# Performance work log

Hardware: AMD Instinct MI355X
Metric: run time of the kernel (lower is better)

## Reference

```python
import jax, jax.numpy as jnp
import numpy as np

E = 8       # num experts
T = 1024    # num tokens
H = 1024    # hidden dim
I = 1024    # intermediate dim (per gate/up half)


def setup_inputs() -> dict:
    key = jax.random.key(0)
    k1, k2, k3, k4 = jax.random.split(key, 4)
    return {
        "hidden_states": jax.random.normal(k1, (T, H), jnp.float32),
        "router_logits": jax.random.normal(k2, (T, E), jnp.float32),
        # W13 stored pre-transposed as in the module: [E, H, 2*I]
        "W13": jax.random.normal(k3, (E, H, 2 * I), jnp.float32) * 0.02,
        # W2 stored pre-transposed: [E, I, H]
        "W2": jax.random.normal(k4, (E, I, H), jnp.float32) * 0.02,
        "top_k": 2,
    }


def reference(hidden_states, router_logits, W13, W2, top_k):
    num_experts = router_logits.shape[-1]
    # --- routing: topk_softmax (softmax over all experts, then top-k) ---
    probs = jax.nn.softmax(router_logits, axis=-1)            # [T, E]
    w, idx = jax.lax.top_k(probs, top_k)                      # [T, K]
    # renormalize=True path of moe_gather
    w = w / jnp.sum(w, axis=-1, keepdims=True)
    # combine weights per expert: [T, E]
    combine = jnp.sum(jax.nn.one_hot(idx, num_experts, dtype=w.dtype) * w[..., None], axis=1)
    # --- grouped gate-up GEMM + silu_and_mul ---
    h13 = jnp.einsum('th,ehf->tef', hidden_states, W13)       # [T, E, 2I]
    gate, up = jnp.split(h13, 2, axis=-1)                     # each [T, E, I]
    act = jax.nn.silu(gate) * up                              # silu_and_mul
    # --- grouped down GEMM ---
    down = jnp.einsum('tei,eih->teh', act, W2)                # [T, E, H]
    # --- combine (moe_gather) ---
    return jnp.einsum('te,teh->th', combine, down)            # [T, H]
```

## Files before the change

kernel.cpp:

```cpp
#include <hip/hip_runtime.h>
#include <stdint.h>

#define NE    8
#define NTOK  1024
#define NH    1024
#define NI    1024
#define N13   2048

#define PREP_BLOCKS 6657
#define G1MAX       768
#define G2MAX       768

typedef __attribute__((ext_vector_type(8))) short short8;
typedef __attribute__((ext_vector_type(4))) float f32x4;
typedef unsigned short u16;
typedef unsigned int   u32;

__device__ __forceinline__ u16 f2bf(float x) {
    union { float f; u32 u; } v; v.f = x;
    return (u16)((v.u + 0x7fffu + ((v.u >> 16) & 1u)) >> 16);
}
__device__ __forceinline__ u32 cvt_pk(float lo, float hi) {
    u32 r;
    asm("v_cvt_pk_bf16_f32 %0, %1, %2" : "=v"(r) : "v"(lo), "v"(hi));
    return r;
}
__device__ __forceinline__ void async_ld16(u16* lds, const u16* g) {
    __builtin_amdgcn_global_load_lds(
        (const __attribute__((address_space(1))) u32*)g,
        (__attribute__((address_space(3))) u32*)lds, 16, 0, 0);
}

__device__ __forceinline__ bool find_tile(
    const int* __restrict__ counts, int tile, int bm, int ntn,
    int& e_o, int& mt_o, int& nt_o, int& cnt_o, int& base_o)
{
    int base = 0;
    #pragma unroll
    for (int e = 0; e < NE; e++) {
        const int cnt = counts[e];
        const int mtiles = (cnt + bm - 1) / bm;
        const int tiles = mtiles * ntn;
        if (tile < tiles) {
            e_o = e; mt_o = tile / ntn; nt_o = tile - (tile / ntn) * ntn;
            cnt_o = cnt; base_o = base; return true;
        }
        tile -= tiles; base += cnt;
    }
    return false;
}

#define SYNCV(N)                                                           \
    {                                                                      \
        asm volatile("s_waitcnt vmcnt(" #N ") lgkmcnt(0)" ::: "memory");   \
        __builtin_amdgcn_s_barrier();                                      \
        __builtin_amdgcn_sched_barrier(0);                                 \
    }

__global__ __launch_bounds__(256) void prep_kernel(
    const float* __restrict__ X, const float* __restrict__ logits,
    const float* __restrict__ W13, const float* __restrict__ W2,
    int* __restrict__ counts, int* __restrict__ pair_tok,
    int* __restrict__ inv, float* __restrict__ tokw,
    u16* __restrict__ Xb, u16* __restrict__ W13t, u16* __restrict__ W2t)
{
    __shared__ __align__(16) float Ts[64][65];
    const int tid = threadIdx.x;
    const int b = blockIdx.x;

    if (b == 0) {
        int* s_cnt  = (int*)&Ts[0][0];
        int* s_base = s_cnt + NE;
        if (tid < NE) s_cnt[tid] = 0;
        __syncthreads();
        int eA[4][2]; int slotA[4][2]; float wA[4][2];
        #pragma unroll
        for (int i = 0; i < 4; i++) {
            const int t = tid * 4 + i;
            float l[NE];
            #pragma unroll
            for (int e = 0; e < NE; e++) l[e] = logits[t * NE + e];
            int i0 = 0;
            #pragma unroll
            for (int e = 1; e < NE; e++) if (l[e] > l[i0]) i0 = e;
            int i1 = -1;
            #pragma unroll
            for (int e = 0; e < NE; e++) {
                if (e == i0) continue;
                if (i1 < 0 || l[e] > l[i1]) i1 = e;
            }
            const float e10 = __expf(l[i1] - l[i0]);
            const float invw = 1.0f / (1.0f + e10);
            eA[i][0] = i0; eA[i][1] = i1;
            wA[i][0] = invw; wA[i][1] = e10 * invw;
            slotA[i][0] = atomicAdd(&s_cnt[i0], 1);
            slotA[i][1] = atomicAdd(&s_cnt[i1], 1);
        }
        __syncthreads();
        if (tid == 0) {
            int acc = 0;
            #pragma unroll
            for (int e = 0; e < NE; e++) { s_base[e] = acc; acc += s_cnt[e]; }
        }
        __syncthreads();
        if (tid < NE) counts[tid] = s_cnt[tid];
        #pragma unroll
        for (int i = 0; i < 4; i++) {
            const int t = tid * 4 + i;
            #pragma unroll
            for (int k = 0; k < 2; k++) {
                const int p = s_base[eA[i][k]] + slotA[i][k];
                pair_tok[p] = t;
                inv[t * 2 + k] = p;
                tokw[t * 2 + k] = wA[i][k];
            }
        }
    } else if (b <= 512) {
        const int i = (b - 1) * 256 + tid;
        const float4* s = (const float4*)X;
        const float4 a = s[2 * i], c = s[2 * i + 1];
        uint4 o;
        o.x = cvt_pk(a.x, a.y);
        o.y = cvt_pk(a.z, a.w);
        o.z = cvt_pk(c.x, c.y);
        o.w = cvt_pk(c.z, c.w);
        *(uint4*)(Xb + (size_t)i * 8) = o;
    } else {
        const int wb = b - 513;
        const float* src; u16* dst; int K, N, tb;
        if (wb < 4096) { src = W13; dst = W13t; K = NH; N = N13; tb = wb; }
        else           { src = W2;  dst = W2t;  K = NI; N = NH;  tb = wb - 4096; }
        const int ktiles = K >> 6, ntiles = N >> 6;
        const int tpe = ktiles * ntiles;
        const int e = tb / tpe;
        const int rem = tb - e * tpe;
        const int kt = rem / ntiles, ntl = rem - (rem / ntiles) * ntiles;
        const float* sb = src + ((size_t)e * K + (size_t)kt * 64) * N + ntl * 64;
        #pragma unroll
        for (int i = 0; i < 4; i++) {
            const int idx = tid + i * 256;
            const int r = idx >> 4, c = (idx & 15) << 2;
            const float4 v = *(const float4*)(sb + (size_t)r * N + c);
            Ts[r][c + 0] = v.x; Ts[r][c + 1] = v.y;
            Ts[r][c + 2] = v.z; Ts[r][c + 3] = v.w;
        }
        __syncthreads();
        u16* db = dst + ((size_t)e * N + (size_t)ntl * 64) * K + kt * 64;
        #pragma unroll
        for (int i = 0; i < 2; i++) {
            const int u = tid + i * 256;
            const int n = u >> 3, k8 = (u & 7) << 3;
            uint4 o;
            o.x = cvt_pk(Ts[k8 + 0][n], Ts[k8 + 1][n]);
            o.y = cvt_pk(Ts[k8 + 2][n], Ts[k8 + 3][n]);
            o.z = cvt_pk(Ts[k8 + 4][n], Ts[k8 + 5][n]);
            o.w = cvt_pk(Ts[k8 + 6][n], Ts[k8 + 7][n]);
            *(uint4*)(db + (size_t)n * K + k8) = o;
        }
    }
}

__global__ __launch_bounds__(256, 3) void gemm1_kernel(
    const u16* __restrict__ Xb, const u16* __restrict__ W13t,
    const int* __restrict__ counts, const int* __restrict__ pair_tok,
    u16* __restrict__ act)
{
    int e, mt, nt, cnt, base;
    if (!find_tile(counts, blockIdx.x, 128, 32, e, mt, nt, cnt, base)) return;

    __shared__ __align__(16) u16 As[4][128 * 32];
    __shared__ __align__(16) u16 Bs[4][64 * 32];

    const int tid = threadIdx.x;
    const int ct  = nt * 32;

    const int sc = (((tid & 3) ^ ((tid >> 3) & 3)) << 3);
    const int rr = tid >> 2;
    const int tok0 = pair_tok[base + min(mt * 128 + rr,      cnt - 1)];
    const int tok1 = pair_tok[base + min(mt * 128 + 64 + rr, cnt - 1)];
    const u16* ga0 = Xb + (size_t)tok0 * NH + sc;
    const u16* ga1 = Xb + (size_t)tok1 * NH + sc;
    const int wcol = (rr < 32) ? (ct + rr) : (NI + ct + rr - 32);
    const u16* gb  = W13t + ((size_t)e * N13 + wcol) * NH + sc;

    const int lane = tid & 63, w = tid >> 6;
    const int quad = lane >> 4, lid = lane & 15;
    const int rw = w >> 1, cw = w & 1;
    int aoff[4];
    #pragma unroll
    for (int mi = 0; mi < 4; mi++) {
        const int row = rw * 64 + mi * 16 + lid;
        aoff[mi] = row * 32 + ((quad ^ ((row >> 1) & 3)) << 3);
    }
    int bgoff, buoff;
    { const int n = cw * 16 + lid;
      bgoff = n * 32 + ((quad ^ ((n >> 1) & 3)) << 3); }
    { const int n = 32 + cw * 16 + lid;
      buoff = n * 32 + ((quad ^ ((n >> 1) & 3)) << 3); }

    f32x4 accg[4] = {};
    f32x4 accu[4] = {};

#define STAGE1(S, K)                                                       \
    {                                                                      \
        async_ld16(&As[S][tid * 8],         ga0 + (K));                    \
        async_ld16(&As[S][(256 + tid) * 8], ga1 + (K));                    \
        async_ld16(&Bs[S][tid * 8],         gb  + (K));                    \
    }
#define COMP1(S)                                                           \
    {                                                                      \
        const short8 gv = *(const short8*)&Bs[S][bgoff];                   \
        const short8 uv = *(const short8*)&Bs[S][buoff];                   \
        __builtin_amdgcn_s_setprio(1);                                     \
        _Pragma("unroll") for (int mi = 0; mi < 4; mi++) {                 \
            const short8 av = *(const short8*)&As[S][aoff[mi]];            \
            accg[mi] = __builtin_amdgcn_mfma_f32_16x16x32_bf16(            \
                av, gv, accg[mi], 0, 0, 0);                                \
            accu[mi] = __builtin_amdgcn_mfma_f32_16x16x32_bf16(            \
                av, uv, accu[mi], 0, 0, 0);                                \
        }                                                                  \
        __builtin_amdgcn_s_setprio(0);                                     \
    }
#define STEP1(J, NV)                                                       \
    SYNCV(NV)                                                              \
    if ((J) + 3 < 32) { STAGE1((((J) + 3) & 3), (((J) + 3) * 32)) }        \
    COMP1(((J) & 3))

    STAGE1(0, 0)
    STAGE1(1, 32)
    STAGE1(2, 64)

    STEP1(0, 6)  STEP1(1, 6)  STEP1(2, 6)  STEP1(3, 6)
    STEP1(4, 6)  STEP1(5, 6)  STEP1(6, 6)  STEP1(7, 6)
    STEP1(8, 6)  STEP1(9, 6)  STEP1(10, 6) STEP1(11, 6)
    STEP1(12, 6) STEP1(13, 6) STEP1(14, 6) STEP1(15, 6)
    STEP1(16, 6) STEP1(17, 6) STEP1(18, 6) STEP1(19, 6)
    STEP1(20, 6) STEP1(21, 6) STEP1(22, 6) STEP1(23, 6)
    STEP1(24, 6) STEP1(25, 6) STEP1(26, 6) STEP1(27, 6)
    STEP1(28, 6) STEP1(29, 6) STEP1(30, 3) STEP1(31, 0)

    const int col = ct + cw * 16 + lid;
    #pragma unroll
    for (int mi = 0; mi < 4; mi++) {
        #pragma unroll
        for (int r = 0; r < 4; r++) {
            const int row = mt * 128 + rw * 64 + mi * 16 + quad * 4 + r;
            if (row < cnt) {
                const float g = accg[mi][r], u = accu[mi][r];
                act[(size_t)(base + row) * NI + col] =
                    f2bf(g / (1.0f + __expf(-g)) * u);
            }
        }
    }
#undef STAGE1
#undef COMP1
#undef STEP1
}

__global__ __launch_bounds__(256, 3) void gemm2_kernel(
    const u16* __restrict__ act, const u16* __restrict__ W2t,
    const int* __restrict__ counts,
    float* __restrict__ down0, float* __restrict__ down1)
{
    int e, mt, ntq, cnt, base;
    if (!find_tile(counts, blockIdx.x, 128, 32, e, mt, ntq, cnt, base)) return;
    const int kh = ntq & 1;
    const int nt = ntq >> 1;
    const int ct = nt * 64;
    const int kbase = kh * 512;
    float* __restrict__ dwn = kh ? down1 : down0;

    __shared__ __align__(16) u16 As[4][128 * 32];
    __shared__ __align__(16) u16 Bs[4][64 * 32];

    const int tid = threadIdx.x;

    const int sc = (((tid & 3) ^ ((tid >> 3) & 3)) << 3);
    const int rr = tid >> 2;
    const int p0 = base + min(mt * 128 + rr,      cnt - 1);
    const int p1 = base + min(mt * 128 + 64 + rr, cnt - 1);
    const u16* ga0 = act + (size_t)p0 * NI + kbase + sc;
    const u16* ga1 = act + (size_t)p1 * NI + kbase + sc;
    const u16* gb  = W2t + ((size_t)e * NH + ct + rr) * NI + kbase + sc;

    const int lane = tid & 63, w = tid >> 6;
    const int quad = lane >> 4, lid = lane & 15;
    const int rw = w >> 1, cw = w & 1;
    int aoff[4], boff[2];
    #pragma unroll
    for (int mi = 0; mi < 4; mi++) {
        const int row = rw * 64 + mi * 16 + lid;
        aoff[mi] = row * 32 + ((quad ^ ((row >> 1) & 3)) << 3);
    }
    #pragma unroll
    for (int nj = 0; nj < 2; nj++) {
        const int n = cw * 32 + nj * 16 + lid;
        boff[nj] = n * 32 + ((quad ^ ((n >> 1) & 3)) << 3);
    }

    f32x4 acc[4][2] = {};

#define STAGE2(S, K)                                                       \
    {                                                                      \
        async_ld16(&As[S][tid * 8],         ga0 + (K));                    \
        async_ld16(&As[S][(256 + tid) * 8], ga1 + (K));                    \
        async_ld16(&Bs[S][tid * 8],         gb  + (K));                    \
    }
#define COMP2(S)                                                           \
    {                                                                      \
        const short8 bv0 = *(const short8*)&Bs[S][boff[0]];                \
        const short8 bv1 = *(const short8*)&Bs[S][boff[1]];                \
        __builtin_amdgcn_s_setprio(1);                                     \
        _Pragma("unroll") for (int mi = 0; mi < 4; mi++) {                 \
            const short8 av = *(const short8*)&As[S][aoff[mi]];            \
            acc[mi][0] = __builtin_amdgcn_mfma_f32_16x16x32_bf16(          \
                av, bv0, acc[mi][0], 0, 0, 0);                             \
            acc[mi][1] = __builtin_amdgcn_mfma_f32_16x16x32_bf16(          \
                av, bv1, acc[mi][1], 0, 0, 0);                             \
        }                                                                  \
        __builtin_amdgcn_s_setprio(0);                                     \
    }
#define STEP2(J, NV)                                                       \
    SYNCV(NV)                                                              \
    if ((J) + 3 < 16) { STAGE2((((J) + 3) & 3), (((J) + 3) * 32)) }        \
    COMP2(((J) & 3))

    STAGE2(0, 0)
    STAGE2(1, 32)
    STAGE2(2, 64)

    STEP2(0, 6)  STEP2(1, 6)  STEP2(2, 6)  STEP2(3, 6)
    STEP2(4, 6)  STEP2(5, 6)  STEP2(6, 6)  STEP2(7, 6)
    STEP2(8, 6)  STEP2(9, 6)  STEP2(10, 6) STEP2(11, 6)
    STEP2(12, 6) STEP2(13, 6) STEP2(14, 3) STEP2(15, 0)

    #pragma unroll
    for (int mi = 0; mi < 4; mi++) {
        #pragma unroll
        for (int r = 0; r < 4; r++) {
            const int row = mt * 128 + rw * 64 + mi * 16 + quad * 4 + r;
            if (row < cnt) {
                #pragma unroll
                for (int nj = 0; nj < 2; nj++) {
                    dwn[(size_t)(base + row) * NH + ct + cw * 32 + nj * 16 + lid] =
                        acc[mi][nj][r];
                }
            }
        }
    }
#undef STAGE2
#undef COMP2
#undef STEP2
}

__global__ __launch_bounds__(256) void combine_kernel(
    const float* __restrict__ down0, const float* __restrict__ down1,
    const int* __restrict__ inv, const float* __restrict__ tokw,
    float* __restrict__ out)
{
    const int t = blockIdx.x;
    const int p0 = inv[2 * t], p1 = inv[2 * t + 1];
    const float w0 = tokw[2 * t], w1 = tokw[2 * t + 1];
    const int i = threadIdx.x * 4;
    const float4 a0 = *(const float4*)(down0 + (size_t)p0 * NH + i);
    const float4 a1 = *(const float4*)(down1 + (size_t)p0 * NH + i);
    const float4 b0 = *(const float4*)(down0 + (size_t)p1 * NH + i);
    const float4 b1 = *(const float4*)(down1 + (size_t)p1 * NH + i);
    float4 o;
    o.x = w0 * (a0.x + a1.x) + w1 * (b0.x + b1.x);
    o.y = w0 * (a0.y + a1.y) + w1 * (b0.y + b1.y);
    o.z = w0 * (a0.z + a1.z) + w1 * (b0.z + b1.z);
    o.w = w0 * (a0.w + a1.w) + w1 * (b0.w + b1.w);
    *(float4*)(out + (size_t)t * NH + i) = o;
}

extern "C" void kernel_launch(void* const* d_in, const int* in_sizes, int n_in,
                              void* d_out, int out_size, void* d_ws, size_t ws_size,
                              hipStream_t stream)
{
    const float* X      = (const float*)d_in[0];
    const float* logits = (const float*)d_in[1];
    const float* W13    = (const float*)d_in[2];
    const float* W2     = (const float*)d_in[3];
    float* out = (float*)d_out;

    char* ws = (char*)d_ws;
    int*   counts   = (int*)(ws + 0);
    int*   pair_tok = (int*)(ws + 1024);
    int*   inv      = (int*)(ws + 16384);
    float* tokw     = (float*)(ws + 32768);
    u16*   Xb       = (u16*)(ws + 65536);
    u16*   act      = (u16*)(ws + (size_t)4  * 1024 * 1024);
    float* down0    = (float*)(ws + (size_t)8  * 1024 * 1024);
    float* down1    = (float*)(ws + (size_t)16 * 1024 * 1024);
    u16*   W13t     = (u16*)(ws + (size_t)24 * 1024 * 1024);
    u16*   W2t      = (u16*)(ws + (size_t)56 * 1024 * 1024);

    prep_kernel<<<PREP_BLOCKS, 256, 0, stream>>>(
        X, logits, W13, W2, counts, pair_tok, inv, tokw, Xb, W13t, W2t);
    gemm1_kernel<<<G1MAX, 256, 0, stream>>>(Xb, W13t, counts, pair_tok, act);
    gemm2_kernel<<<G2MAX, 256, 0, stream>>>(act, W2t, counts, down0, down1);
    combine_kernel<<<NTOK, 256, 0, stream>>>(down0, down1, inv, tokw, out);
}
```

Baseline: 171.7 us.

## Fuse fp32 weight conversion into GEMM B-tile loads, dropping the prep transpose pass

Removes the per-call prep stage that transposed and converted the W13 and W2 weights to bf16. Instead, each GEMM loads fp32 weight rows into registers one stage ahead, converts them with cvt_pk and writes them to swizzled LDS inside the pipelined K-loop. This targets the extra full read and write of the weight tensors in prep. In exchange the GEMMs fetch twice the bytes per B tile, hold more registers, and use a new staging schedule with adjusted waitcnt values.

```diff
diff --git a/kernel.cpp b/kernel.cpp
--- a/kernel.cpp
+++ b/kernel.cpp
@@ -7,7 +7,7 @@
 #define NI    1024
 #define N13   2048
 
-#define PREP_BLOCKS 6657
+#define PREP_BLOCKS 513
 #define G1MAX       768
 #define G2MAX       768
 
@@ -50,6 +50,8 @@
     return false;
 }
 
+#define SB __builtin_amdgcn_sched_barrier(0);
+
 #define SYNCV(N)                                                           \
     {                                                                      \
         asm volatile("s_waitcnt vmcnt(" #N ") lgkmcnt(0)" ::: "memory");   \
@@ -59,18 +61,16 @@
 
 __global__ __launch_bounds__(256) void prep_kernel(
     const float* __restrict__ X, const float* __restrict__ logits,
-    const float* __restrict__ W13, const float* __restrict__ W2,
     int* __restrict__ counts, int* __restrict__ pair_tok,
     int* __restrict__ inv, float* __restrict__ tokw,
-    u16* __restrict__ Xb, u16* __restrict__ W13t, u16* __restrict__ W2t)
-{
-    __shared__ __align__(16) float Ts[64][65];
+    u16* __restrict__ Xb)
+{
+    __shared__ int s_cnt[NE];
+    __shared__ int s_base[NE];
     const int tid = threadIdx.x;
     const int b = blockIdx.x;
 
     if (b == 0) {
-        int* s_cnt  = (int*)&Ts[0][0];
-        int* s_base = s_cnt + NE;
         if (tid < NE) s_cnt[tid] = 0;
         __syncthreads();
         int eA[4][2]; int slotA[4][2]; float wA[4][2];
@@ -115,7 +115,7 @@
                 tokw[t * 2 + k] = wA[i][k];
             }
         }
-    } else if (b <= 512) {
+    } else {
         const int i = (b - 1) * 256 + tid;
         const float4* s = (const float4*)X;
         const float4 a = s[2 * i], c = s[2 * i + 1];
@@ -125,43 +125,11 @@
         o.z = cvt_pk(c.x, c.y);
         o.w = cvt_pk(c.z, c.w);
         *(uint4*)(Xb + (size_t)i * 8) = o;
-    } else {
-        const int wb = b - 513;
-        const float* src; u16* dst; int K, N, tb;
-        if (wb < 4096) { src = W13; dst = W13t; K = NH; N = N13; tb = wb; }
-        else           { src = W2;  dst = W2t;  K = NI; N = NH;  tb = wb - 4096; }
-        const int ktiles = K >> 6, ntiles = N >> 6;
-        const int tpe = ktiles * ntiles;
-        const int e = tb / tpe;
-        const int rem = tb - e * tpe;
-        const int kt = rem / ntiles, ntl = rem - (rem / ntiles) * ntiles;
-        const float* sb = src + ((size_t)e * K + (size_t)kt * 64) * N + ntl * 64;
-        #pragma unroll
-        for (int i = 0; i < 4; i++) {
-            const int idx = tid + i * 256;
-            const int r = idx >> 4, c = (idx & 15) << 2;
-            const float4 v = *(const float4*)(sb + (size_t)r * N + c);
-            Ts[r][c + 0] = v.x; Ts[r][c + 1] = v.y;
-            Ts[r][c + 2] = v.z; Ts[r][c + 3] = v.w;
-        }
-        __syncthreads();
-        u16* db = dst + ((size_t)e * N + (size_t)ntl * 64) * K + kt * 64;
-        #pragma unroll
-        for (int i = 0; i < 2; i++) {
-            const int u = tid + i * 256;
-            const int n = u >> 3, k8 = (u & 7) << 3;
-            uint4 o;
-            o.x = cvt_pk(Ts[k8 + 0][n], Ts[k8 + 1][n]);
-            o.y = cvt_pk(Ts[k8 + 2][n], Ts[k8 + 3][n]);
-            o.z = cvt_pk(Ts[k8 + 4][n], Ts[k8 + 5][n]);
-            o.w = cvt_pk(Ts[k8 + 6][n], Ts[k8 + 7][n]);
-            *(uint4*)(db + (size_t)n * K + k8) = o;
-        }
     }
 }
 
 __global__ __launch_bounds__(256, 3) void gemm1_kernel(
-    const u16* __restrict__ Xb, const u16* __restrict__ W13t,
+    const u16* __restrict__ Xb, const float* __restrict__ W13,
     const int* __restrict__ counts, const int* __restrict__ pair_tok,
     u16* __restrict__ act)
 {
@@ -180,8 +148,17 @@
     const int tok1 = pair_tok[base + min(mt * 128 + 64 + rr, cnt - 1)];
     const u16* ga0 = Xb + (size_t)tok0 * NH + sc;
     const u16* ga1 = Xb + (size_t)tok1 * NH + sc;
-    const int wcol = (rr < 32) ? (ct + rr) : (NI + ct + rr - 32);
-    const u16* gb  = W13t + ((size_t)e * N13 + wcol) * NH + sc;
+
+    const int n0 = (tid & 15) << 2;
+    const int kp = tid >> 4;
+    const int f0 = (n0 < 32) ? (ct + n0) : (NI + ct + n0 - 32);
+    const float* gw = W13 + ((size_t)e * NH + 2 * kp) * N13 + f0;
+    int wboff[4];
+    #pragma unroll
+    for (int jj = 0; jj < 4; jj++) {
+        const int n = n0 + jj;
+        wboff[jj] = n * 32 + (((kp >> 2) ^ ((n >> 1) & 3)) << 3) + ((kp & 3) << 1);
+    }
 
     const int lane = tid & 63, w = tid >> 6;
     const int quad = lane >> 4, lid = lane & 15;
@@ -200,13 +177,22 @@
 
     f32x4 accg[4] = {};
     f32x4 accu[4] = {};
-
-#define STAGE1(S, K)                                                       \
+    float4 bq[4][2];
+
+#define ISSUEA1(S, K)                                                      \
     {                                                                      \
         async_ld16(&As[S][tid * 8],         ga0 + (K));                    \
         async_ld16(&As[S][(256 + tid) * 8], ga1 + (K));                    \
-        async_ld16(&Bs[S][tid * 8],         gb  + (K));                    \
-    }
+    }
+#define LOADB1(RB, K)                                                      \
+    { bq[RB][0] = *(const float4*)(gw + (size_t)(K) * N13);                \
+      bq[RB][1] = *(const float4*)(gw + (size_t)(K) * N13 + N13); }
+#define WRB1(S, RB)                                                        \
+    { _Pragma("unroll") for (int jj = 0; jj < 4; jj++) {                   \
+        *(u32*)&Bs[S][wboff[jj]] =                                         \
+            cvt_pk(((const float*)&bq[RB][0])[jj],                         \
+                   ((const float*)&bq[RB][1])[jj]);                        \
+    } }
 #define COMP1(S)                                                           \
     {                                                                      \
         const short8 gv = *(const short8*)&Bs[S][bgoff];                   \
@@ -223,21 +209,31 @@
     }
 #define STEP1(J, NV)                                                       \
     SYNCV(NV)                                                              \
-    if ((J) + 3 < 32) { STAGE1((((J) + 3) & 3), (((J) + 3) * 32)) }        \
-    COMP1(((J) & 3))
-
-    STAGE1(0, 0)
-    STAGE1(1, 32)
-    STAGE1(2, 64)
-
-    STEP1(0, 6)  STEP1(1, 6)  STEP1(2, 6)  STEP1(3, 6)
-    STEP1(4, 6)  STEP1(5, 6)  STEP1(6, 6)  STEP1(7, 6)
-    STEP1(8, 6)  STEP1(9, 6)  STEP1(10, 6) STEP1(11, 6)
-    STEP1(12, 6) STEP1(13, 6) STEP1(14, 6) STEP1(15, 6)
-    STEP1(16, 6) STEP1(17, 6) STEP1(18, 6) STEP1(19, 6)
-    STEP1(20, 6) STEP1(21, 6) STEP1(22, 6) STEP1(23, 6)
-    STEP1(24, 6) STEP1(25, 6) STEP1(26, 6) STEP1(27, 6)
-    STEP1(28, 6) STEP1(29, 6) STEP1(30, 3) STEP1(31, 0)
+    if ((J) + 3 < 32) { ISSUEA1((((J) + 3) & 3), (((J) + 3) * 32)) }       \
+    SB                                                                     \
+    if ((J) + 4 < 32) { LOADB1((((J) + 4) & 3), (((J) + 4) * 32)) }        \
+    SB                                                                     \
+    COMP1(((J) & 3))                                                       \
+    SB                                                                     \
+    if ((J) + 1 < 32) { WRB1((((J) + 1) & 3), (((J) + 1) & 3)) }
+
+    LOADB1(0, 0)    SB
+    ISSUEA1(0, 0)   SB
+    LOADB1(1, 32)   SB
+    ISSUEA1(1, 32)  SB
+    LOADB1(2, 64)   SB
+    ISSUEA1(2, 64)  SB
+    LOADB1(3, 96)   SB
+    WRB1(0, 0)
+
+    STEP1(0, 10)  STEP1(1, 10)  STEP1(2, 10)  STEP1(3, 10)
+    STEP1(4, 10)  STEP1(5, 10)  STEP1(6, 10)  STEP1(7, 10)
+    STEP1(8, 10)  STEP1(9, 10)  STEP1(10, 10) STEP1(11, 10)
+    STEP1(12, 10) STEP1(13, 10) STEP1(14, 10) STEP1(15, 10)
+    STEP1(16, 10) STEP1(17, 10) STEP1(18, 10) STEP1(19, 10)
+    STEP1(20, 10) STEP1(21, 10) STEP1(22, 10) STEP1(23, 10)
+    STEP1(24, 10) STEP1(25, 10) STEP1(26, 10) STEP1(27, 10)
+    STEP1(28, 10) STEP1(29, 8)  STEP1(30, 4)  STEP1(31, 0)
 
     const int col = ct + cw * 16 + lid;
     #pragma unroll
@@ -252,13 +248,15 @@
             }
         }
     }
-#undef STAGE1
+#undef ISSUEA1
+#undef LOADB1
+#undef WRB1
 #undef COMP1
 #undef STEP1
 }
 
 __global__ __launch_bounds__(256, 3) void gemm2_kernel(
-    const u16* __restrict__ act, const u16* __restrict__ W2t,
+    const u16* __restrict__ act, const float* __restrict__ W2,
     const int* __restrict__ counts,
     float* __restrict__ down0, float* __restrict__ down1)
 {
@@ -281,7 +279,16 @@
     const int p1 = base + min(mt * 128 + 64 + rr, cnt - 1);
     const u16* ga0 = act + (size_t)p0 * NI + kbase + sc;
     const u16* ga1 = act + (size_t)p1 * NI + kbase + sc;
-    const u16* gb  = W2t + ((size_t)e * NH + ct + rr) * NI + kbase + sc;
+
+    const int n0 = (tid & 15) << 2;
+    const int kp = tid >> 4;
+    const float* gw = W2 + ((size_t)e * NI + kbase + 2 * kp) * NH + ct + n0;
+    int wboff[4];
+    #pragma unroll
+    for (int jj = 0; jj < 4; jj++) {
+        const int n = n0 + jj;
+        wboff[jj] = n * 32 + (((kp >> 2) ^ ((n >> 1) & 3)) << 3) + ((kp & 3) << 1);
+    }
 
     const int lane = tid & 63, w = tid >> 6;
     const int quad = lane >> 4, lid = lane & 15;
@@ -299,13 +306,22 @@
     }
 
     f32x4 acc[4][2] = {};
-
-#define STAGE2(S, K)                                                       \
+    float4 bq[4][2];
+
+#define ISSUEA2(S, K)                                                      \
     {                                                                      \
         async_ld16(&As[S][tid * 8],         ga0 + (K));                    \
         async_ld16(&As[S][(256 + tid) * 8], ga1 + (K));                    \
-        async_ld16(&Bs[S][tid * 8],         gb  + (K));                    \
-    }
+    }
+#define LOADB2(RB, K)                                                      \
+    { bq[RB][0] = *(const float4*)(gw + (size_t)(K) * NH);                 \
+      bq[RB][1] = *(const float4*)(gw + (size_t)(K) * NH + NH); }
+#define WRB2(S, RB)                                                        \
+    { _Pragma("unroll") for (int jj = 0; jj < 4; jj++) {                   \
+        *(u32*)&Bs[S][wboff[jj]] =                                         \
+            cvt_pk(((const float*)&bq[RB][0])[jj],                         \
+                   ((const float*)&bq[RB][1])[jj]);                        \
+    } }
 #define COMP2(S)                                                           \
     {                                                                      \
         const short8 bv0 = *(const short8*)&Bs[S][boff[0]];                \
@@ -322,17 +338,27 @@
     }
 #define STEP2(J, NV)                                                       \
     SYNCV(NV)                                                              \
-    if ((J) + 3 < 16) { STAGE2((((J) + 3) & 3), (((J) + 3) * 32)) }        \
-    COMP2(((J) & 3))
-
-    STAGE2(0, 0)
-    STAGE2(1, 32)
-    STAGE2(2, 64)
-
-    STEP2(0, 6)  STEP2(1, 6)  STEP2(2, 6)  STEP2(3, 6)
-    STEP2(4, 6)  STEP2(5, 6)  STEP2(6, 6)  STEP2(7, 6)
-    STEP2(8, 6)  STEP2(9, 6)  STEP2(10, 6) STEP2(11, 6)
-    STEP2(12, 6) STEP2(13, 6) STEP2(14, 3) STEP2(15, 0)
+    if ((J) + 3 < 16) { ISSUEA2((((J) + 3) & 3), (((J) + 3) * 32)) }       \
+    SB                                                                     \
+    if ((J) + 4 < 16) { LOADB2((((J) + 4) & 3), (((J) + 4) * 32)) }        \
+    SB                                                                     \
+    COMP2(((J) & 3))                                                       \
+    SB                                                                     \
+    if ((J) + 1 < 16) { WRB2((((J) + 1) & 3), (((J) + 1) & 3)) }
+
+    LOADB2(0, 0)    SB
+    ISSUEA2(0, 0)   SB
+    LOADB2(1, 32)   SB
+    ISSUEA2(1, 32)  SB
+    LOADB2(2, 64)   SB
+    ISSUEA2(2, 64)  SB
+    LOADB2(3, 96)   SB
+    WRB2(0, 0)
+
+    STEP2(0, 10)  STEP2(1, 10)  STEP2(2, 10)  STEP2(3, 10)
+    STEP2(4, 10)  STEP2(5, 10)  STEP2(6, 10)  STEP2(7, 10)
+    STEP2(8, 10)  STEP2(9, 10)  STEP2(10, 10) STEP2(11, 10)
+    STEP2(12, 10) STEP2(13, 8)  STEP2(14, 4)  STEP2(15, 0)
 
     #pragma unroll
     for (int mi = 0; mi < 4; mi++) {
@@ -348,7 +374,9 @@
             }
         }
     }
-#undef STAGE2
+#undef ISSUEA2
+#undef LOADB2
+#undef WRB2
 #undef COMP2
 #undef STEP2
 }
@@ -393,12 +421,10 @@
     u16*   act      = (u16*)(ws + (size_t)4  * 1024 * 1024);
     float* down0    = (float*)(ws + (size_t)8  * 1024 * 1024);
     float* down1    = (float*)(ws + (size_t)16 * 1024 * 1024);
-    u16*   W13t     = (u16*)(ws + (size_t)24 * 1024 * 1024);
-    u16*   W2t      = (u16*)(ws + (size_t)56 * 1024 * 1024);
 
     prep_kernel<<<PREP_BLOCKS, 256, 0, stream>>>(
-        X, logits, W13, W2, counts, pair_tok, inv, tokw, Xb, W13t, W2t);
-    gemm1_kernel<<<G1MAX, 256, 0, stream>>>(Xb, W13t, counts, pair_tok, act);
-    gemm2_kernel<<<G2MAX, 256, 0, stream>>>(act, W2t, counts, down0, down1);
+        X, logits, counts, pair_tok, inv, tokw, Xb);
+    gemm1_kernel<<<G1MAX, 256, 0, stream>>>(Xb, W13, counts, pair_tok, act);
+    gemm2_kernel<<<G2MAX, 256, 0, stream>>>(act, W2, counts, down0, down1);
     combine_kernel<<<NTOK, 256, 0, stream>>>(down0, down1, inv, tokw, out);
 }
```

New measurement: 185.4 us. 7.9% more time.

## Double N-tile width in both expert GEMMs to raise operand reuse

Applied to the files above, without the earlier changes.

Both grouped GEMMs move from 128x64 tiles to 128x128 tiles: gemm1 now covers 64 gate plus 64 up columns per block, and gemm2 covers 128 output columns. The tile count per expert is halved, the max grid sizes drop to match, and the vmcnt wait counts are adjusted for four async loads per stage. Each warp now does twice the MFMAs per LDS load of A, which reduces global and LDS traffic per FLOP. In exchange, accumulator registers double and occupancy is lowered from 3 to 2 blocks per CU, leaving fewer blocks to fill the GPU.

```diff
diff --git a/kernel.cpp b/kernel.cpp
--- a/kernel.cpp
+++ b/kernel.cpp
@@ -8,8 +8,8 @@
 #define N13   2048
 
 #define PREP_BLOCKS 6657
-#define G1MAX       768
-#define G2MAX       768
+#define G1MAX       384
+#define G2MAX       384
 
 typedef __attribute__((ext_vector_type(8))) short short8;
 typedef __attribute__((ext_vector_type(4))) float f32x4;
@@ -160,19 +160,19 @@
     }
 }
 
-__global__ __launch_bounds__(256, 3) void gemm1_kernel(
+__global__ __launch_bounds__(256, 2) void gemm1_kernel(
     const u16* __restrict__ Xb, const u16* __restrict__ W13t,
     const int* __restrict__ counts, const int* __restrict__ pair_tok,
     u16* __restrict__ act)
 {
     int e, mt, nt, cnt, base;
-    if (!find_tile(counts, blockIdx.x, 128, 32, e, mt, nt, cnt, base)) return;
+    if (!find_tile(counts, blockIdx.x, 128, 16, e, mt, nt, cnt, base)) return;
 
     __shared__ __align__(16) u16 As[4][128 * 32];
-    __shared__ __align__(16) u16 Bs[4][64 * 32];
+    __shared__ __align__(16) u16 Bs[4][128 * 32];
 
     const int tid = threadIdx.x;
-    const int ct  = nt * 32;
+    const int ct  = nt * 64;
 
     const int sc = (((tid & 3) ^ ((tid >> 3) & 3)) << 3);
     const int rr = tid >> 2;
@@ -180,8 +180,8 @@
     const int tok1 = pair_tok[base + min(mt * 128 + 64 + rr, cnt - 1)];
     const u16* ga0 = Xb + (size_t)tok0 * NH + sc;
     const u16* ga1 = Xb + (size_t)tok1 * NH + sc;
-    const int wcol = (rr < 32) ? (ct + rr) : (NI + ct + rr - 32);
-    const u16* gb  = W13t + ((size_t)e * N13 + wcol) * NH + sc;
+    const u16* gb0 = W13t + ((size_t)e * N13 + ct + rr) * NH + sc;
+    const u16* gb1 = W13t + ((size_t)e * N13 + NI + ct + rr) * NH + sc;
 
     const int lane = tid & 63, w = tid >> 6;
     const int quad = lane >> 4, lid = lane & 15;
@@ -192,32 +192,41 @@
         const int row = rw * 64 + mi * 16 + lid;
         aoff[mi] = row * 32 + ((quad ^ ((row >> 1) & 3)) << 3);
     }
-    int bgoff, buoff;
-    { const int n = cw * 16 + lid;
-      bgoff = n * 32 + ((quad ^ ((n >> 1) & 3)) << 3); }
-    { const int n = 32 + cw * 16 + lid;
-      buoff = n * 32 + ((quad ^ ((n >> 1) & 3)) << 3); }
-
-    f32x4 accg[4] = {};
-    f32x4 accu[4] = {};
+    int bgoff[2], buoff[2];
+    #pragma unroll
+    for (int nj = 0; nj < 2; nj++) {
+        const int ng = cw * 32 + nj * 16 + lid;
+        bgoff[nj] = ng * 32 + ((quad ^ ((ng >> 1) & 3)) << 3);
+        const int nu = 64 + cw * 32 + nj * 16 + lid;
+        buoff[nj] = nu * 32 + ((quad ^ ((nu >> 1) & 3)) << 3);
+    }
+
+    f32x4 accg[4][2] = {};
+    f32x4 accu[4][2] = {};
 
 #define STAGE1(S, K)                                                       \
     {                                                                      \
         async_ld16(&As[S][tid * 8],         ga0 + (K));                    \
         async_ld16(&As[S][(256 + tid) * 8], ga1 + (K));                    \
-        async_ld16(&Bs[S][tid * 8],         gb  + (K));                    \
+        async_ld16(&Bs[S][tid * 8],         gb0 + (K));                    \
+        async_ld16(&Bs[S][(256 + tid) * 8], gb1 + (K));                    \
     }
 #define COMP1(S)                                                           \
     {                                                                      \
-        const short8 gv = *(const short8*)&Bs[S][bgoff];                   \
-        const short8 uv = *(const short8*)&Bs[S][buoff];                   \
+        short8 gv[2], uv[2];                                               \
+        _Pragma("unroll") for (int nj = 0; nj < 2; nj++) {                 \
+            gv[nj] = *(const short8*)&Bs[S][bgoff[nj]];                    \
+            uv[nj] = *(const short8*)&Bs[S][buoff[nj]];                    \
+        }                                                                  \
         __builtin_amdgcn_s_setprio(1);                                     \
         _Pragma("unroll") for (int mi = 0; mi < 4; mi++) {                 \
             const short8 av = *(const short8*)&As[S][aoff[mi]];            \
-            accg[mi] = __builtin_amdgcn_mfma_f32_16x16x32_bf16(            \
-                av, gv, accg[mi], 0, 0, 0);                                \
-            accu[mi] = __builtin_amdgcn_mfma_f32_16x16x32_bf16(            \
-                av, uv, accu[mi], 0, 0, 0);                                \
+            _Pragma("unroll") for (int nj = 0; nj < 2; nj++) {             \
+                accg[mi][nj] = __builtin_amdgcn_mfma_f32_16x16x32_bf16(    \
+                    av, gv[nj], accg[mi][nj], 0, 0, 0);                    \
+                accu[mi][nj] = __builtin_amdgcn_mfma_f32_16x16x32_bf16(    \
+                    av, uv[nj], accu[mi][nj], 0, 0, 0);                    \
+            }                                                              \
         }                                                                  \
         __builtin_amdgcn_s_setprio(0);                                     \
     }
@@ -230,25 +239,28 @@
     STAGE1(1, 32)
     STAGE1(2, 64)
 
-    STEP1(0, 6)  STEP1(1, 6)  STEP1(2, 6)  STEP1(3, 6)
-    STEP1(4, 6)  STEP1(5, 6)  STEP1(6, 6)  STEP1(7, 6)
-    STEP1(8, 6)  STEP1(9, 6)  STEP1(10, 6) STEP1(11, 6)
-    STEP1(12, 6) STEP1(13, 6) STEP1(14, 6) STEP1(15, 6)
-    STEP1(16, 6) STEP1(17, 6) STEP1(18, 6) STEP1(19, 6)
-    STEP1(20, 6) STEP1(21, 6) STEP1(22, 6) STEP1(23, 6)
-    STEP1(24, 6) STEP1(25, 6) STEP1(26, 6) STEP1(27, 6)
-    STEP1(28, 6) STEP1(29, 6) STEP1(30, 3) STEP1(31, 0)
-
-    const int col = ct + cw * 16 + lid;
+    STEP1(0, 8)  STEP1(1, 8)  STEP1(2, 8)  STEP1(3, 8)
+    STEP1(4, 8)  STEP1(5, 8)  STEP1(6, 8)  STEP1(7, 8)
+    STEP1(8, 8)  STEP1(9, 8)  STEP1(10, 8) STEP1(11, 8)
+    STEP1(12, 8) STEP1(13, 8) STEP1(14, 8) STEP1(15, 8)
+    STEP1(16, 8) STEP1(17, 8) STEP1(18, 8) STEP1(19, 8)
+    STEP1(20, 8) STEP1(21, 8) STEP1(22, 8) STEP1(23, 8)
+    STEP1(24, 8) STEP1(25, 8) STEP1(26, 8) STEP1(27, 8)
+    STEP1(28, 8) STEP1(29, 8) STEP1(30, 4) STEP1(31, 0)
+
     #pragma unroll
     for (int mi = 0; mi < 4; mi++) {
         #pragma unroll
         for (int r = 0; r < 4; r++) {
             const int row = mt * 128 + rw * 64 + mi * 16 + quad * 4 + r;
             if (row < cnt) {
-                const float g = accg[mi][r], u = accu[mi][r];
-                act[(size_t)(base + row) * NI + col] =
-                    f2bf(g / (1.0f + __expf(-g)) * u);
+                #pragma unroll
+                for (int nj = 0; nj < 2; nj++) {
+                    const float g = accg[mi][nj][r], u = accu[mi][nj][r];
+                    const int col = ct + cw * 32 + nj * 16 + lid;
+                    act[(size_t)(base + row) * NI + col] =
+                        f2bf(g / (1.0f + __expf(-g)) * u);
+                }
             }
         }
     }
@@ -257,21 +269,21 @@
 #undef STEP1
 }
 
-__global__ __launch_bounds__(256, 3) void gemm2_kernel(
+__global__ __launch_bounds__(256, 2) void gemm2_kernel(
     const u16* __restrict__ act, const u16* __restrict__ W2t,
     const int* __restrict__ counts,
     float* __restrict__ down0, float* __restrict__ down1)
 {
     int e, mt, ntq, cnt, base;
-    if (!find_tile(counts, blockIdx.x, 128, 32, e, mt, ntq, cnt, base)) return;
+    if (!find_tile(counts, blockIdx.x, 128, 16, e, mt, ntq, cnt, base)) return;
     const int kh = ntq & 1;
     const int nt = ntq >> 1;
-    const int ct = nt * 64;
+    const int ct = nt * 128;
     const int kbase = kh * 512;
     float* __restrict__ dwn = kh ? down1 : down0;
 
     __shared__ __align__(16) u16 As[4][128 * 32];
-    __shared__ __align__(16) u16 Bs[4][64 * 32];
+    __shared__ __align__(16) u16 Bs[4][128 * 32];
 
     const int tid = threadIdx.x;
 
@@ -281,42 +293,44 @@
     const int p1 = base + min(mt * 128 + 64 + rr, cnt - 1);
     const u16* ga0 = act + (size_t)p0 * NI + kbase + sc;
     const u16* ga1 = act + (size_t)p1 * NI + kbase + sc;
-    const u16* gb  = W2t + ((size_t)e * NH + ct + rr) * NI + kbase + sc;
+    const u16* gb0 = W2t + ((size_t)e * NH + ct + rr)      * NI + kbase + sc;
+    const u16* gb1 = W2t + ((size_t)e * NH + ct + 64 + rr) * NI + kbase + sc;
 
     const int lane = tid & 63, w = tid >> 6;
     const int quad = lane >> 4, lid = lane & 15;
     const int rw = w >> 1, cw = w & 1;
-    int aoff[4], boff[2];
+    int aoff[4], boff[4];
     #pragma unroll
     for (int mi = 0; mi < 4; mi++) {
         const int row = rw * 64 + mi * 16 + lid;
         aoff[mi] = row * 32 + ((quad ^ ((row >> 1) & 3)) << 3);
     }
     #pragma unroll
-    for (int nj = 0; nj < 2; nj++) {
-        const int n = cw * 32 + nj * 16 + lid;
+    for (int nj = 0; nj < 4; nj++) {
+        const int n = cw * 64 + nj * 16 + lid;
         boff[nj] = n * 32 + ((quad ^ ((n >> 1) & 3)) << 3);
     }
 
-    f32x4 acc[4][2] = {};
+    f32x4 acc[4][4] = {};
 
 #define STAGE2(S, K)                                                       \
     {                                                                      \
         async_ld16(&As[S][tid * 8],         ga0 + (K));                    \
         async_ld16(&As[S][(256 + tid) * 8], ga1 + (K));                    \
-        async_ld16(&Bs[S][tid * 8],         gb  + (K));                    \
+        async_ld16(&Bs[S][tid * 8],         gb0 + (K));                    \
+        async_ld16(&Bs[S][(256 + tid) * 8], gb1 + (K));                    \
     }
 #define COMP2(S)                                                           \
     {                                                                      \
-        const short8 bv0 = *(const short8*)&Bs[S][boff[0]];                \
-        const short8 bv1 = *(const short8*)&Bs[S][boff[1]];                \
+        short8 bv[4];                                                      \
+        _Pragma("unroll") for (int nj = 0; nj < 4; nj++)                   \
+            bv[nj] = *(const short8*)&Bs[S][boff[nj]];                     \
         __builtin_amdgcn_s_setprio(1);                                     \
         _Pragma("unroll") for (int mi = 0; mi < 4; mi++) {                 \
             const short8 av = *(const short8*)&As[S][aoff[mi]];            \
-            acc[mi][0] = __builtin_amdgcn_mfma_f32_16x16x32_bf16(          \
-                av, bv0, acc[mi][0], 0, 0, 0);                             \
-            acc[mi][1] = __builtin_amdgcn_mfma_f32_16x16x32_bf16(          \
-                av, bv1, acc[mi][1], 0, 0, 0);                             \
+            _Pragma("unroll") for (int nj = 0; nj < 4; nj++)               \
+                acc[mi][nj] = __builtin_amdgcn_mfma_f32_16x16x32_bf16(     \
+                    av, bv[nj], acc[mi][nj], 0, 0, 0);                     \
         }                                                                  \
         __builtin_amdgcn_s_setprio(0);                                     \
     }
@@ -329,10 +343,10 @@
     STAGE2(1, 32)
     STAGE2(2, 64)
 
-    STEP2(0, 6)  STEP2(1, 6)  STEP2(2, 6)  STEP2(3, 6)
-    STEP2(4, 6)  STEP2(5, 6)  STEP2(6, 6)  STEP2(7, 6)
-    STEP2(8, 6)  STEP2(9, 6)  STEP2(10, 6) STEP2(11, 6)
-    STEP2(12, 6) STEP2(13, 6) STEP2(14, 3) STEP2(15, 0)
+    STEP2(0, 8)  STEP2(1, 8)  STEP2(2, 8)  STEP2(3, 8)
+    STEP2(4, 8)  STEP2(5, 8)  STEP2(6, 8)  STEP2(7, 8)
+    STEP2(8, 8)  STEP2(9, 8)  STEP2(10, 8) STEP2(11, 8)
+    STEP2(12, 8) STEP2(13, 8) STEP2(14, 4) STEP2(15, 0)
 
     #pragma unroll
     for (int mi = 0; mi < 4; mi++) {
@@ -341,9 +355,9 @@
             const int row = mt * 128 + rw * 64 + mi * 16 + quad * 4 + r;
             if (row < cnt) {
                 #pragma unroll
-                for (int nj = 0; nj < 2; nj++) {
-                    dwn[(size_t)(base + row) * NH + ct + cw * 32 + nj * 16 + lid] =
-                        acc[mi][nj][r];
+                for (int nj = 0; nj < 4; nj++) {
+                    const int col = ct + cw * 64 + nj * 16 + lid;
+                    dwn[(size_t)(base + row) * NH + col] = acc[mi][nj][r];
                 }
             }
         }
```

Result: no change. 172.4 us (+0.4%).
